# Optimization experiments

Hardware: AMD Instinct MI355X
Metric: run time of the kernel (lower is better)

The kernel has to match this reference:

```python
import jax, jax.numpy as jnp
import numpy as np

B, N, HID, H, M = 4, 16384, 512, 8, 32
D = HID // H  # 64


def setup_inputs() -> dict:
    key = jax.random.key(0)
    ks = jax.random.split(key, 8)
    s = 0.02
    return {
        "x": jax.random.normal(ks[0], (B, N, HID), jnp.float32),
        "wkv": jax.random.normal(ks[1], (2 * HID, HID), jnp.float32) * s,
        "bkv": jnp.zeros((2 * HID,), jnp.float32),
        "wtq": jax.random.normal(ks[2], (H, M, D), jnp.float32) * s,
        "alpha1": jnp.ones((H,), jnp.float32),
        "mix1_w": jax.random.normal(ks[3], (H * M, H * M), jnp.float32) * (1.0 / np.sqrt(H * M)),
        "ln1_w": jnp.ones((D,), jnp.float32),
        "ln1_b": jnp.zeros((D,), jnp.float32),
        "wqkv": jax.random.normal(ks[4], (3 * HID, HID), jnp.float32) * s,
        "wout": jax.random.normal(ks[5], (HID, HID), jnp.float32) * s,
        "bout": jnp.zeros((HID,), jnp.float32),
    }


def _layernorm(x, w, b, eps=1e-5):
    mu = x.mean(-1, keepdims=True)
    var = ((x - mu) ** 2).mean(-1, keepdims=True)
    return (x - mu) * jax.lax.rsqrt(var + eps) * w + b


def reference(x, wkv, bkv, wtq, alpha1, mix1_w, ln1_w, ln1_b, wqkv, wout, bout):
    # key/value projection: [B, N, 2*HID]
    kv = x @ wkv.T + bkv
    xk, xv = jnp.split(kv, 2, axis=-1)
    xk = xk.reshape(B, N, H, D).transpose(0, 2, 1, 3)  # b h n d
    xv = xv.reshape(B, N, H, D).transpose(0, 2, 1, 3)
    # slice scores + 1x1 conv head-mixing over the (H*M) channel dim
    scores = jnp.einsum('hmd,bhnd->bhmn', wtq, xk)
    scores = jnp.einsum('oc,bcn->bon', mix1_w, scores.reshape(B, H * M, N)).reshape(B, H, M, N)
    # softmax over the slice dim M (dim=-2)
    sw = jax.nn.softmax(scores * alpha1[:, None, None], axis=-2)  # b h m n
    # weighted reduction to slice tokens, normalized by total weight per slice
    tok = jnp.einsum('bhmn,bhnd->bhmd', sw, xv)
    tok = tok / (sw.sum(axis=-1, keepdims=True) + 1e-5)
    tok = _layernorm(tok, ln1_w, ln1_b)
    tok = tok.transpose(0, 2, 1, 3).reshape(B, M, HID)  # b m (h d)
    # small inner MHA over the M=32 slice tokens
    qkv = tok @ wqkv.T
    q, k, v = jnp.split(qkv, 3, axis=-1)
    q = q.reshape(B, M, H, D).transpose(0, 2, 1, 3)
    k = k.reshape(B, M, H, D).transpose(0, 2, 1, 3)
    v = v.reshape(B, M, H, D).transpose(0, 2, 1, 3)
    dots = jnp.einsum('bhqd,bhkd->bhqk', q, k) * (D ** -0.5)
    attn = jax.nn.softmax(dots, axis=-1)
    out_tok = jnp.einsum('bhqk,bhkd->bhqd', attn, v)
    # broadcast slice tokens back to the N points via slice weights
    out = jnp.einsum('bhmd,bhmn->bhnd', out_tok, sw)
    out = out.transpose(0, 2, 1, 3).reshape(B, N, HID)
    out = out @ wout.T + bout
    return (out, sw, alpha1[:, None, None], jnp.zeros((H, M), jnp.float32), attn)
```

## Files before the change

### kernel.cpp

```cpp
#include <hip/hip_runtime.h>
#include <hip/hip_bf16.h>

#define B_ 4
#define N_ 16384
#define HID_ 512
#define H_ 8
#define M_ 32
#define D_ 64
#define HM_ 256

typedef __hip_bfloat16 bf16;
typedef __bf16 bf16x8 __attribute__((ext_vector_type(8)));
typedef float f32x4 __attribute__((ext_vector_type(4)));

__device__ __forceinline__ void gl_lds16(const bf16* g, bf16* l) {
    __builtin_amdgcn_global_load_lds(
        (const __attribute__((address_space(1))) void*)g,
        (__attribute__((address_space(3))) void*)l, 16, 0, 0);
}

__device__ __forceinline__ int xcd_swz(int lin, int nwg) {
    return (lin & 7) * (nwg >> 3) + (lin >> 3);
}

__device__ __forceinline__ uint bpk(float lo, float hi) {
    bf16 a = __float2bfloat16(lo), b = __float2bfloat16(hi);
    return (uint)(*(ushort*)&a) | ((uint)(*(ushort*)&b) << 16);
}

__device__ __forceinline__ void stage_tile_lin(const bf16* __restrict__ G, long long r0,
        int kk, int ld, bf16* lds, int t) {
    const int l = t & 63, w = t >> 6;
    const int srow = l >> 3;
    const int skel = (l & 7) * 8;
#pragma unroll
    for (int j = 0; j < 4; ++j) {
        int q = j * 4 + w;
        gl_lds16(G + (r0 + q * 8 + srow) * (long long)ld + kk + skel, lds + q * 512);
    }
}

__device__ __forceinline__ void mfma_core(
        const bf16* __restrict__ Ag, const bf16* __restrict__ Bg,
        long long arow0, int bcol0, int lda, int ldb, int kiters,
        bf16* As, bf16* Bs, f32x4 acc[4][4]) {
    const int t = threadIdx.x;
    const int l = t & 63, w = t >> 6;
    const int wm = w >> 1, wn = w & 1;
    for (int kt = 0; kt < kiters; ++kt) {
        const int kk = kt * 64;
        stage_tile_lin(Ag, arow0, kk, lda, As, t);
        stage_tile_lin(Bg, bcol0, kk, ldb, Bs, t);
        __syncthreads();
#pragma unroll
        for (int ks = 0; ks < 64; ks += 32) {
            bf16x8 af[4], bfr[4];
#pragma unroll
            for (int mf = 0; mf < 4; ++mf)
                af[mf] = *(const bf16x8*)(As + (wm * 64 + mf * 16 + (l & 15)) * 64 + ks + (l >> 4) * 8);
#pragma unroll
            for (int nf = 0; nf < 4; ++nf)
                bfr[nf] = *(const bf16x8*)(Bs + (wn * 64 + nf * 16 + (l & 15)) * 64 + ks + (l >> 4) * 8);
#pragma unroll
            for (int mf = 0; mf < 4; ++mf)
#pragma unroll
                for (int nf = 0; nf < 4; ++nf)
                    acc[mf][nf] = __builtin_amdgcn_mfma_f32_16x16x32_bf16(af[mf], bfr[nf], acc[mf][nf], 0, 0, 0);
        }
        __syncthreads();
    }
}

__global__ __launch_bounds__(256) void k_cast4(const float* __restrict__ s,
        ushort* __restrict__ d) {
    long long i = (long long)blockIdx.x * 256 + threadIdx.x;
    float4 v = reinterpret_cast<const float4*>(s)[i];
    ushort4 o;
    bf16 a0 = __float2bfloat16(v.x), a1 = __float2bfloat16(v.y);
    bf16 a2 = __float2bfloat16(v.z), a3 = __float2bfloat16(v.w);
    o.x = *(ushort*)&a0; o.y = *(ushort*)&a1; o.z = *(ushort*)&a2; o.w = *(ushort*)&a3;
    reinterpret_cast<ushort4*>(d)[i] = o;
}

__global__ __launch_bounds__(256) void k_wfused(const float* __restrict__ mix1,
        const float* __restrict__ wtq, float* __restrict__ wf) {
    const int idx = blockIdx.x * 256 + threadIdx.x;
    const int o = idx >> 9, k = idx & 511;
    const int h = k >> 6, dd = k & 63;
    float s = 0.f;
#pragma unroll
    for (int m = 0; m < 32; ++m)
        s += mix1[(long long)o * 256 + h * 32 + m] * wtq[((long long)h * 32 + m) * 64 + dd];
    wf[(long long)o * 512 + k] = s;
}

__global__ __launch_bounds__(256) void k_wsc(const float* __restrict__ wf,
        const float* __restrict__ wkv, const float* __restrict__ bkv,
        const float* __restrict__ alpha1, bf16* __restrict__ wv_sc,
        float* __restrict__ bias768) {
    __shared__ float wfrow[512];
    __shared__ float red[256];
    const int o = blockIdx.x, t = threadIdx.x;
    wfrow[t] = wf[(long long)o * 512 + t];
    wfrow[t + 256] = wf[(long long)o * 512 + 256 + t];
    __syncthreads();
    const float al = alpha1[o >> 5];
    float a0 = 0.f, a1 = 0.f;
    for (int c = 0; c < 512; ++c) {
        float wv = wfrow[c];
        a0 += wv * wkv[(long long)c * 512 + t];
        a1 += wv * wkv[(long long)c * 512 + t + 256];
    }
    wv_sc[(long long)(512 + o) * 512 + t] = __float2bfloat16(a0 * al);
    wv_sc[(long long)(512 + o) * 512 + t + 256] = __float2bfloat16(a1 * al);
    float p = wfrow[t] * bkv[t] + wfrow[t + 256] * bkv[t + 256];
    red[t] = p; __syncthreads();
    for (int s = 128; s >= 1; s >>= 1) {
        if (t < s) red[t] += red[t + s];
        __syncthreads();
    }
    if (t == 0) bias768[512 + o] = red[0] * al;
}

__global__ __launch_bounds__(256) void k_prep(const float* __restrict__ bkv,
        float* __restrict__ bias768) {
    int j = blockIdx.x * 256 + threadIdx.x;
    bias768[j] = bkv[512 + j];
}

__global__ __launch_bounds__(256) void k12_mfma(const bf16* __restrict__ xb,
        const bf16* __restrict__ wv_sc, const float* __restrict__ bias768,
        bf16* __restrict__ xv, float* __restrict__ swout,
        bf16* __restrict__ sw_bt, float* __restrict__ part) {
    __shared__ __align__(16) bf16 smem[16384];
    bf16* As = smem;
    bf16* Bs = smem + 8192;
    f32x4 acc[4][4];
#pragma unroll
    for (int i = 0; i < 4; ++i)
#pragma unroll
        for (int j = 0; j < 4; ++j) acc[i][j] = (f32x4)(0.0f);
    const int wg = xcd_swz(blockIdx.y * 6 + blockIdx.x, 3072);
    const int bx = wg % 6, by = wg / 6;
    const long long arow0 = (long long)by * 128;
    const int bcol0 = bx * 128;
    mfma_core(xb, wv_sc, arow0, bcol0, 512, 512, 8, As, Bs, acc);

    const int t = threadIdx.x;
    const int l = t & 63, w = t >> 6, wm = w >> 1, wn = w & 1;
    const int l15 = l & 15, lq = l >> 4;
#pragma unroll
    for (int nf = 0; nf < 4; ++nf) {
        float bv = bias768[bcol0 + wn * 64 + nf * 16 + l15];
#pragma unroll
        for (int mf = 0; mf < 4; ++mf)
#pragma unroll
            for (int r = 0; r < 4; ++r) acc[mf][nf][r] += bv;
    }

    if (bcol0 >= 512) {
#pragma unroll
        for (int mf = 0; mf < 4; ++mf)
#pragma unroll
            for (int r = 0; r < 4; ++r)
#pragma unroll
                for (int g = 0; g < 2; ++g) {
                    float v0 = acc[mf][2 * g][r], v1 = acc[mf][2 * g + 1][r];
                    float mx = fmaxf(v0, v1);
#pragma unroll
                    for (int mk = 1; mk <= 8; mk <<= 1) mx = fmaxf(mx, __shfl_xor(mx, mk));
                    float e0 = __expf(v0 - mx), e1 = __expf(v1 - mx);
                    float s = e0 + e1;
#pragma unroll
                    for (int mk = 1; mk <= 8; mk <<= 1) s += __shfl_xor(s, mk);
                    float ri = 1.f / s;
                    acc[mf][2 * g][r] = e0 * ri;
                    acc[mf][2 * g + 1][r] = e1 * ri;
                }
        {
            float* cpart = (float*)smem;
#pragma unroll
            for (int nf = 0; nf < 4; ++nf) {
                float ps = 0.f;
#pragma unroll
                for (int mf = 0; mf < 4; ++mf)
#pragma unroll
                    for (int r = 0; r < 4; ++r) ps += acc[mf][nf][r];
                ps += __shfl_xor(ps, 16);
                ps += __shfl_xor(ps, 32);
                if (lq == 0) cpart[wm * 128 + wn * 64 + nf * 16 + l15] = ps;
            }
            __syncthreads();
            if (t < 128)
                part[(long long)by * 256 + (bcol0 - 512) + t] = cpart[t] + cpart[128 + t];
        }
        const int b = (int)(arow0 >> 14);
        const int nbase = (int)(arow0 & 16383) + wm * 64;
#pragma unroll
        for (int mf = 0; mf < 4; ++mf) {
            long long rowb = arow0 + wm * 64 + mf * 16 + lq * 4;
#pragma unroll
            for (int nf = 0; nf < 4; ++nf) {
                int cglob = (bcol0 - 512) + wn * 64 + nf * 16 + l15;
                float4 v = {acc[mf][nf][0], acc[mf][nf][1], acc[mf][nf][2], acc[mf][nf][3]};
                *reinterpret_cast<float4*>(swout + ((long long)b * HM_ + cglob) * N_
                                           + nbase + mf * 16 + lq * 4) = v;
#pragma unroll
                for (int r = 0; r < 4; ++r)
                    sw_bt[(rowb + r) * 256 + cglob] = __float2bfloat16(acc[mf][nf][r]);
            }
        }
    } else {
#pragma unroll
        for (int mf = 0; mf < 4; ++mf) {
            long long rowb = arow0 + wm * 64 + mf * 16 + lq * 4;
#pragma unroll
            for (int nf = 0; nf < 4; ++nf) {
                int col = bcol0 + wn * 64 + nf * 16 + l15;
#pragma unroll
                for (int r = 0; r < 4; ++r)
                    xv[(rowb + r) * 512 + col] = __float2bfloat16(acc[mf][nf][r]);
            }
        }
    }
}

__global__ __launch_bounds__(256) void k3_tok(const bf16* __restrict__ sw_bt,
        const bf16* __restrict__ xv, float* __restrict__ tok_part) {
    __shared__ __align__(16) float smem[17408];
    float (*swsT)[36] = reinterpret_cast<float(*)[36]>(smem);
    bf16* xvs = reinterpret_cast<bf16*>(smem + 9216);
    const int t = threadIdx.x;
    const int chunk = blockIdx.x;
    const int bh = blockIdx.y;
    const int n0 = chunk * 256;
    const int b = bh >> 3, h = bh & 7;
    {
        const long long base = ((long long)(b * N_ + n0 + t)) * 256 + h * 32;
        const uint4* sp = reinterpret_cast<const uint4*>(sw_bt + base);
        uint4 qs[4] = {sp[0], sp[1], sp[2], sp[3]};
        const uint* qu = reinterpret_cast<const uint*>(qs);
#pragma unroll
        for (int j = 0; j < 16; ++j) {
            uint u = qu[j];
            swsT[t][2 * j] = __uint_as_float(u << 16);
            swsT[t][2 * j + 1] = __uint_as_float(u & 0xffff0000u);
        }
    }
    {
        const uint* xg = reinterpret_cast<const uint*>(xv + ((long long)b * N_ + n0) * 512 + h * 64);
        uint* xls = reinterpret_cast<uint*>(xvs);
#pragma unroll
        for (int p = 0; p < 32; ++p) {
            int idx = p * 256 + t;
            int nl = idx >> 5, prt = idx & 31;
            xls[nl * 32 + prt] = xg[(long long)nl * 256 + prt];
        }
    }
    __syncthreads();
    const int l = t & 63, w = t >> 6;
    const int nlh = l >> 5, mtile = (l >> 3) & 3, dtile = l & 7;
    const int m0 = mtile * 8, d0 = dtile * 8;
    float acc[8][8] = {};
    const int wbase = w * 64;
    for (int i = 0; i < 32; ++i) {
        int nl = wbase + i * 2 + nlh;
        float4 s0 = *reinterpret_cast<const float4*>(&swsT[nl][m0]);
        float4 s1 = *reinterpret_cast<const float4*>(&swsT[nl][m0 + 4]);
        uint4 xi = *reinterpret_cast<const uint4*>(&xvs[nl * 64 + d0]);
        float xvf[8];
        xvf[0] = __uint_as_float(xi.x << 16); xvf[1] = __uint_as_float(xi.x & 0xffff0000u);
        xvf[2] = __uint_as_float(xi.y << 16); xvf[3] = __uint_as_float(xi.y & 0xffff0000u);
        xvf[4] = __uint_as_float(xi.z << 16); xvf[5] = __uint_as_float(xi.z & 0xffff0000u);
        xvf[6] = __uint_as_float(xi.w << 16); xvf[7] = __uint_as_float(xi.w & 0xffff0000u);
        float sm[8] = {s0.x, s0.y, s0.z, s0.w, s1.x, s1.y, s1.z, s1.w};
#pragma unroll
        for (int mi = 0; mi < 8; ++mi)
#pragma unroll
            for (int di = 0; di < 8; ++di)
                acc[mi][di] += sm[mi] * xvf[di];
    }
    __syncthreads();
    float* red = smem;
    float* rb = red + (w * 2 + nlh) * 2048;
#pragma unroll
    for (int mi = 0; mi < 8; ++mi) {
        float4 lo = {acc[mi][0], acc[mi][1], acc[mi][2], acc[mi][3]};
        float4 hi = {acc[mi][4], acc[mi][5], acc[mi][6], acc[mi][7]};
        *reinterpret_cast<float4*>(&rb[(m0 + mi) * 64 + d0]) = lo;
        *reinterpret_cast<float4*>(&rb[(m0 + mi) * 64 + d0 + 4]) = hi;
    }
    __syncthreads();
#pragma unroll
    for (int pp = 0; pp < 2; ++pp) {
        int idx4 = pp * 1024 + t * 4;
        float4 s = {0.f, 0.f, 0.f, 0.f};
#pragma unroll
        for (int r = 0; r < 8; ++r) {
            float4 v = *reinterpret_cast<const float4*>(&red[r * 2048 + idx4]);
            s.x += v.x; s.y += v.y; s.z += v.z; s.w += v.w;
        }
        *reinterpret_cast<float4*>(&tok_part[((long long)bh * 64 + chunk) * 2048 + idx4]) = s;
    }
}

__global__ __launch_bounds__(64) void k4a_ln(const float* __restrict__ tok_part,
        const float* __restrict__ part, const float* __restrict__ ln_w,
        const float* __restrict__ ln_b, float* __restrict__ tok_ln) {
    const int bid = blockIdx.x;
    const int bh = bid >> 5, m = bid & 31;
    const int d = threadIdx.x;
    float s = 0.f;
    for (int ch = 0; ch < 64; ++ch)
        s += tok_part[(((long long)bh * 64 + ch) * 32 + m) * 64 + d];
    const int b = bid >> 8, c = bid & 255;
    float ssum = part[((long long)(b * 128 + d)) * 256 + c]
               + part[((long long)(b * 128 + 64 + d)) * 256 + c];
#pragma unroll
    for (int mk = 32; mk >= 1; mk >>= 1) ssum += __shfl_xor(ssum, mk, 64);
    float tokv = s / (ssum + 1e-5f);
    float mu = tokv;
#pragma unroll
    for (int mk = 32; mk >= 1; mk >>= 1) mu += __shfl_xor(mu, mk, 64);
    mu *= (1.f / 64.f);
    float df = tokv - mu;
    float var = df * df;
#pragma unroll
    for (int mk = 32; mk >= 1; mk >>= 1) var += __shfl_xor(var, mk, 64);
    var *= (1.f / 64.f);
    float y = df * rsqrtf(var + 1e-5f) * ln_w[d] + ln_b[d];
    const int bb = bh >> 3, h = bh & 7;
    tok_ln[((long long)bb * 32 + m) * 512 + h * 64 + d] = y;
}

__global__ __launch_bounds__(256) void k_wqT(const float* __restrict__ wq,
        float* __restrict__ wqT) {
    __shared__ float tile[32][33];
    const int k0 = blockIdx.x * 32;
    const int j0 = blockIdx.y * 32;
    const int tx = threadIdx.x & 31, ty = threadIdx.x >> 5;
#pragma unroll
    for (int r = 0; r < 32; r += 8)
        tile[ty + r][tx] = wq[(long long)(j0 + ty + r) * 512 + k0 + tx];
    __syncthreads();
#pragma unroll
    for (int r = 0; r < 32; r += 8)
        wqT[(long long)(k0 + ty + r) * 1536 + j0 + tx] = tile[tx][ty + r];
}

__global__ __launch_bounds__(256) void k4b_qkv(const float* __restrict__ tok_ln,
        const float* __restrict__ wqT, float* __restrict__ qkv) {
    const int j = (blockIdx.x % 6) * 256 + threadIdx.x;
    const int r0 = (blockIdx.x / 6) * 4;
    float a0 = 0, a1 = 0, a2 = 0, a3 = 0;
    for (int k = 0; k < 512; ++k) {
        float wv = wqT[(long long)k * 1536 + j];
        a0 += tok_ln[(r0 + 0) * 512 + k] * wv;
        a1 += tok_ln[(r0 + 1) * 512 + k] * wv;
        a2 += tok_ln[(r0 + 2) * 512 + k] * wv;
        a3 += tok_ln[(r0 + 3) * 512 + k] * wv;
    }
    qkv[(long long)(r0 + 0) * 1536 + j] = a0;
    qkv[(long long)(r0 + 1) * 1536 + j] = a1;
    qkv[(long long)(r0 + 2) * 1536 + j] = a2;
    qkv[(long long)(r0 + 3) * 1536 + j] = a3;
}

__global__ __launch_bounds__(256) void k4c_attn(const float* __restrict__ qkv,
        float* __restrict__ out_tok, float* __restrict__ attn_out) {
    __shared__ float qsT[64][33], ksT[64][33], vsT[64][33];
    __shared__ float att[32][33];
    __shared__ float rinv[32];
    const int t = threadIdx.x;
    const int bid = blockIdx.x;
    const int b = bid >> 3, h = bid & 7;
#pragma unroll
    for (int i = 0; i < 8; ++i) {
        int idx = i * 256 + t;
        int mi = idx >> 6, dd = idx & 63;
        long long base = ((long long)b * 32 + mi) * 1536 + h * 64 + dd;
        qsT[dd][mi] = qkv[base];
        ksT[dd][mi] = qkv[base + 512];
        vsT[dd][mi] = qkv[base + 1024];
    }
    __syncthreads();
#pragma unroll
    for (int i = 0; i < 4; ++i) {
        int idx = i * 256 + t;
        int qi = idx >> 5, ki = idx & 31;
        float s = 0.f;
#pragma unroll
        for (int dd = 0; dd < 64; ++dd) s += qsT[dd][qi] * ksT[dd][ki];
        att[qi][ki] = s * 0.125f;
    }
    __syncthreads();
    if (t < 32) {
        float mx = -1e30f;
        for (int k = 0; k < 32; ++k) mx = fmaxf(mx, att[t][k]);
        float sum = 0.f;
        for (int k = 0; k < 32; ++k) { float e = __expf(att[t][k] - mx); att[t][k] = e; sum += e; }
        rinv[t] = 1.f / sum;
    }
    __syncthreads();
#pragma unroll
    for (int i = 0; i < 4; ++i) {
        int idx = i * 256 + t;
        int qi = idx >> 5, ki = idx & 31;
        float a = att[qi][ki] * rinv[qi];
        att[qi][ki] = a;
        attn_out[(long long)bid * 1024 + qi * 32 + ki] = a;
    }
    __syncthreads();
#pragma unroll
    for (int i = 0; i < 8; ++i) {
        int idx = i * 256 + t;
        int qi = idx >> 6, dd = idx & 63;
        float s = 0.f;
#pragma unroll
        for (int ki = 0; ki < 32; ++ki) s += att[qi][ki] * vsT[dd][ki];
        out_tok[((long long)bid * 32 + qi) * 64 + dd] = s;
    }
}

__global__ __launch_bounds__(256) void k5_w2(const float* __restrict__ wout,
        const float* __restrict__ out_tok, bf16* __restrict__ W2) {
    const int bid = blockIdx.x;
    const int b = bid >> 9, o = bid & 511;
    const int t = threadIdx.x;
    const int h = t >> 5, m = t & 31;
    float s = 0.f;
#pragma unroll
    for (int dd = 0; dd < 64; ++dd)
        s += wout[(long long)o * 512 + h * 64 + dd]
           * out_tok[(((long long)b * 8 + h) * 32 + m) * 64 + dd];
    W2[(long long)bid * 256 + t] = __float2bfloat16(s);
}

__global__ __launch_bounds__(256) void k6_mfma(const bf16* __restrict__ sw_bt,
        const bf16* __restrict__ W2, const float* __restrict__ bout,
        float* __restrict__ out) {
    __shared__ bf16 As[128 * 64], Bs[128 * 64];
    f32x4 acc[4][4];
#pragma unroll
    for (int i = 0; i < 4; ++i)
#pragma unroll
        for (int j = 0; j < 4; ++j) acc[i][j] = (f32x4)(0.0f);
    const int wg = xcd_swz((blockIdx.z * 128 + blockIdx.y) * 4 + blockIdx.x, 2048);
    const int bx = wg & 3, by = (wg >> 2) & 127, bz = wg >> 9;
    const long long arow0 = (long long)by * 128;
    const int bcol0 = bx * 128;
    mfma_core(sw_bt + (long long)bz * N_ * 256, W2 + (long long)bz * 512 * 256,
              arow0, bcol0, 256, 256, 4, As, Bs, acc);
    const int l = threadIdx.x & 63, w = threadIdx.x >> 6;
    const int wm = w >> 1, wn = w & 1;
#pragma unroll
    for (int mf = 0; mf < 4; ++mf) {
#pragma unroll
        for (int nf = 0; nf < 4; ++nf) {
            int col = bcol0 + wn * 64 + nf * 16 + (l & 15);
            float bv = bout[col];
#pragma unroll
            for (int r = 0; r < 4; ++r) {
                long long row = arow0 + wm * 64 + mf * 16 + (l >> 4) * 4 + r;
                out[((long long)bz * N_ + row) * 512 + col] = acc[mf][nf][r] + bv;
            }
        }
    }
}

__global__ void k_misc(const float* __restrict__ alpha1,
        float* __restrict__ outA, float* __restrict__ outZ) {
    int t = threadIdx.x;
    if (t < 8) outA[t] = alpha1[t];
    outZ[t] = 0.f;
}

extern "C" void kernel_launch(void* const* d_in, const int* in_sizes, int n_in,
                              void* d_out, int out_size, void* d_ws, size_t ws_size,
                              hipStream_t stream) {
    const float* x      = (const float*)d_in[0];
    const float* wkv    = (const float*)d_in[1];
    const float* bkv    = (const float*)d_in[2];
    const float* wtq    = (const float*)d_in[3];
    const float* alpha1 = (const float*)d_in[4];
    const float* mix1_w = (const float*)d_in[5];
    const float* ln1_w  = (const float*)d_in[6];
    const float* ln1_b  = (const float*)d_in[7];
    const float* wqkv   = (const float*)d_in[8];
    const float* wout   = (const float*)d_in[9];
    const float* bout   = (const float*)d_in[10];

    float* out    = (float*)d_out;
    float* swout  = out + 33554432LL;
    float* alphaO = out + 50331648LL;
    float* zerosO = out + 50331656LL;
    float* attnO  = out + 50331912LL;

    char* ws = (char*)d_ws;
    bf16*  xb        = (bf16*)(ws);
    float* wqkvT     = (float*)(ws);
    float* wf_f32    = (float*)(ws + 35651584LL);
    float* part      = (float*)(ws + 67108864LL);
    bf16*  sw_bt     = (bf16*)(ws + 100663296LL);
    bf16*  xv        = (bf16*)(ws + 134217728LL);
    float* tok_part  = (float*)(ws + 201326592LL);
    float* tok_ln    = (float*)(ws + 218107904LL);
    float* qkv       = (float*)(ws + 218370048LL);
    float* out_tok   = (float*)(ws + 219156480LL);
    bf16*  W2b       = (bf16*)(ws + 219418624LL);
    bf16*  wv_sc     = (bf16*)(ws + 220467200LL);
    float* bias768   = (float*)(ws + 221253632LL);

    k_cast4<<<256, 256, 0, stream>>>(wkv + 262144, (ushort*)wv_sc);
    k_wfused<<<512, 256, 0, stream>>>(mix1_w, wtq, wf_f32);
    k_wsc<<<256, 256, 0, stream>>>(wf_f32, wkv, bkv, alpha1, wv_sc, bias768);
    k_prep<<<2, 256, 0, stream>>>(bkv, bias768);
    k_cast4<<<32768, 256, 0, stream>>>(x, (ushort*)xb);
    k12_mfma<<<dim3(6, 512), 256, 0, stream>>>(xb, wv_sc, bias768, xv, swout, sw_bt, part);
    k_wqT<<<dim3(16, 48), 256, 0, stream>>>(wqkv, wqkvT);
    k3_tok<<<dim3(64, 32), 256, 0, stream>>>(sw_bt, xv, tok_part);
    k4a_ln<<<1024, 64, 0, stream>>>(tok_part, part, ln1_w, ln1_b, tok_ln);
    k4b_qkv<<<192, 256, 0, stream>>>(tok_ln, wqkvT, qkv);
    k4c_attn<<<32, 256, 0, stream>>>(qkv, out_tok, attnO);
    k5_w2<<<2048, 256, 0, stream>>>(wout, out_tok, W2b);
    k6_mfma<<<dim3(4, 128, 4), 256, 0, stream>>>(sw_bt, W2b, bout, out);
    k_misc<<<1, 256, 0, stream>>>(alpha1, alphaO, zerosO);
}
```

Measured before the change: 361.2 us.

## Double-buffer LDS tiles in k12 GEMM and fold bias prep into k_wsc

Replaces the single-buffered load/sync/compute loop in the k12 projection GEMM with a two-stage ping-pong LDS buffer. The next K tile is staged while MFMAs run on the current one, which aims to hide global-to-LDS latency. LDS per block doubles to 64KB, which may reduce occupancy. The separate k_prep launch is also removed and its bias copy is folded into k_wsc, saving one kernel launch.

Result: faster. 350.4 us (-3.0%).

```diff
diff --git a/kernel.cpp b/kernel.cpp
--- a/kernel.cpp
+++ b/kernel.cpp
@@ -23,11 +23,6 @@
     return (lin & 7) * (nwg >> 3) + (lin >> 3);
 }
 
-__device__ __forceinline__ uint bpk(float lo, float hi) {
-    bf16 a = __float2bfloat16(lo), b = __float2bfloat16(hi);
-    return (uint)(*(ushort*)&a) | ((uint)(*(ushort*)&b) << 16);
-}
-
 __device__ __forceinline__ void stage_tile_lin(const bf16* __restrict__ G, long long r0,
         int kk, int ld, bf16* lds, int t) {
     const int l = t & 63, w = t >> 6;
@@ -37,6 +32,25 @@
     for (int j = 0; j < 4; ++j) {
         int q = j * 4 + w;
         gl_lds16(G + (r0 + q * 8 + srow) * (long long)ld + kk + skel, lds + q * 512);
+    }
+}
+
+__device__ __forceinline__ void mfma_half(const bf16* As, const bf16* Bs,
+        int l, int wm, int wn, f32x4 acc[4][4]) {
+#pragma unroll
+    for (int ks = 0; ks < 64; ks += 32) {
+        bf16x8 af[4], bfr[4];
+#pragma unroll
+        for (int mf = 0; mf < 4; ++mf)
+            af[mf] = *(const bf16x8*)(As + (wm * 64 + mf * 16 + (l & 15)) * 64 + ks + (l >> 4) * 8);
+#pragma unroll
+        for (int nf = 0; nf < 4; ++nf)
+            bfr[nf] = *(const bf16x8*)(Bs + (wn * 64 + nf * 16 + (l & 15)) * 64 + ks + (l >> 4) * 8);
+#pragma unroll
+        for (int mf = 0; mf < 4; ++mf)
+#pragma unroll
+            for (int nf = 0; nf < 4; ++nf)
+                acc[mf][nf] = __builtin_amdgcn_mfma_f32_16x16x32_bf16(af[mf], bfr[nf], acc[mf][nf], 0, 0, 0);
     }
 }
 
@@ -52,21 +66,33 @@
         stage_tile_lin(Ag, arow0, kk, lda, As, t);
         stage_tile_lin(Bg, bcol0, kk, ldb, Bs, t);
         __syncthreads();
-#pragma unroll
-        for (int ks = 0; ks < 64; ks += 32) {
-            bf16x8 af[4], bfr[4];
-#pragma unroll
-            for (int mf = 0; mf < 4; ++mf)
-                af[mf] = *(const bf16x8*)(As + (wm * 64 + mf * 16 + (l & 15)) * 64 + ks + (l >> 4) * 8);
-#pragma unroll
-            for (int nf = 0; nf < 4; ++nf)
-                bfr[nf] = *(const bf16x8*)(Bs + (wn * 64 + nf * 16 + (l & 15)) * 64 + ks + (l >> 4) * 8);
-#pragma unroll
-            for (int mf = 0; mf < 4; ++mf)
-#pragma unroll
-                for (int nf = 0; nf < 4; ++nf)
-                    acc[mf][nf] = __builtin_amdgcn_mfma_f32_16x16x32_bf16(af[mf], bfr[nf], acc[mf][nf], 0, 0, 0);
-        }
+        mfma_half(As, Bs, l, wm, wn, acc);
+        __syncthreads();
+    }
+}
+
+__device__ __forceinline__ void gemm_2ph(
+        const bf16* __restrict__ Ag, const bf16* __restrict__ Bg,
+        long long arow0, int bcol0, int lda, int ldb, int nt,
+        bf16 (*As)[8192], bf16 (*Bs)[8192], f32x4 acc[4][4]) {
+    const int t = threadIdx.x;
+    const int l = t & 63, w = t >> 6;
+    const int wm = w >> 1, wn = w & 1;
+    stage_tile_lin(Ag, arow0, 0, lda, As[0], t);
+    stage_tile_lin(Bg, bcol0, 0, ldb, Bs[0], t);
+    __syncthreads();
+    for (int kt = 0; kt < nt; kt += 2) {
+        if (kt + 1 < nt) {
+            stage_tile_lin(Ag, arow0, (kt + 1) * 64, lda, As[1], t);
+            stage_tile_lin(Bg, bcol0, (kt + 1) * 64, ldb, Bs[1], t);
+        }
+        mfma_half(As[0], Bs[0], l, wm, wn, acc);
+        __syncthreads();
+        if (kt + 2 < nt) {
+            stage_tile_lin(Ag, arow0, (kt + 2) * 64, lda, As[0], t);
+            stage_tile_lin(Bg, bcol0, (kt + 2) * 64, ldb, Bs[0], t);
+        }
+        if (kt + 1 < nt) mfma_half(As[1], Bs[1], l, wm, wn, acc);
         __syncthreads();
     }
 }
@@ -120,21 +146,15 @@
         __syncthreads();
     }
     if (t == 0) bias768[512 + o] = red[0] * al;
-}
-
-__global__ __launch_bounds__(256) void k_prep(const float* __restrict__ bkv,
-        float* __restrict__ bias768) {
-    int j = blockIdx.x * 256 + threadIdx.x;
-    bias768[j] = bkv[512 + j];
+    if (t < 2) bias768[o * 2 + t] = bkv[512 + o * 2 + t];
 }
 
 __global__ __launch_bounds__(256) void k12_mfma(const bf16* __restrict__ xb,
         const bf16* __restrict__ wv_sc, const float* __restrict__ bias768,
         bf16* __restrict__ xv, float* __restrict__ swout,
         bf16* __restrict__ sw_bt, float* __restrict__ part) {
-    __shared__ __align__(16) bf16 smem[16384];
-    bf16* As = smem;
-    bf16* Bs = smem + 8192;
+    __shared__ __align__(16) bf16 As[2][8192];
+    __shared__ __align__(16) bf16 Bs[2][8192];
     f32x4 acc[4][4];
 #pragma unroll
     for (int i = 0; i < 4; ++i)
@@ -144,7 +164,7 @@
     const int bx = wg % 6, by = wg / 6;
     const long long arow0 = (long long)by * 128;
     const int bcol0 = bx * 128;
-    mfma_core(xb, wv_sc, arow0, bcol0, 512, 512, 8, As, Bs, acc);
+    gemm_2ph(xb, wv_sc, arow0, bcol0, 512, 512, 8, As, Bs, acc);
 
     const int t = threadIdx.x;
     const int l = t & 63, w = t >> 6, wm = w >> 1, wn = w & 1;
@@ -178,7 +198,7 @@
                     acc[mf][2 * g + 1][r] = e1 * ri;
                 }
         {
-            float* cpart = (float*)smem;
+            float* cpart = (float*)&As[0][0];
 #pragma unroll
             for (int nf = 0; nf < 4; ++nf) {
                 float ps = 0.f;
@@ -514,7 +534,6 @@
     k_cast4<<<256, 256, 0, stream>>>(wkv + 262144, (ushort*)wv_sc);
     k_wfused<<<512, 256, 0, stream>>>(mix1_w, wtq, wf_f32);
     k_wsc<<<256, 256, 0, stream>>>(wf_f32, wkv, bkv, alpha1, wv_sc, bias768);
-    k_prep<<<2, 256, 0, stream>>>(bkv, bias768);
     k_cast4<<<32768, 256, 0, stream>>>(x, (ushort*)xb);
     k12_mfma<<<dim3(6, 512), 256, 0, stream>>>(xb, wv_sc, bias768, xv, swout, sw_bt, part);
     k_wqT<<<dim3(16, 48), 256, 0, stream>>>(wqkv, wqkvT);
```
